# Performance work log

Measured on AMD Instinct MI355X. Metric: run time of the kernel, lower is better.

The kernel has to match this reference:

```python
import jax, jax.numpy as jnp
import numpy as np

DIM = 2048
N_HEADS = 16
KV_HEADS = 2
HEAD_DIM = DIM // N_HEADS
N_REP = N_HEADS // KV_HEADS
EPS = 1e-6


def rms_norm(x, weight):
    # norm over last dim in float32, cast back (inputs already fp32 here)
    xf = x.astype(jnp.float32)
    n = xf * jax.lax.rsqrt(jnp.mean(xf * xf, axis=-1, keepdims=True) + EPS)
    return (weight * n).astype(x.dtype)


def rotate_half(x):
    x1, x2 = jnp.split(x, 2, axis=-1)
    return jnp.concatenate((-x2, x1), axis=-1)


def apply_rotary(x, cos, sin):
    return x * cos + rotate_half(x) * sin


def setup_inputs() -> dict:
    key = jax.random.key(0)
    ks = jax.random.split(key, 8)
    B, S = 2, 2048
    x = jax.random.normal(ks[0], (B, S, DIM), dtype=jnp.float32)
    cos = jax.random.uniform(ks[1], (1, 1, S, HEAD_DIM), dtype=jnp.float32)
    sin = jax.random.uniform(ks[2], (1, 1, S, HEAD_DIM), dtype=jnp.float32)
    scale = 0.02
    wq = jax.random.normal(ks[3], (N_HEADS * HEAD_DIM, DIM), dtype=jnp.float32) * scale
    wk = jax.random.normal(ks[4], (KV_HEADS * HEAD_DIM, DIM), dtype=jnp.float32) * scale
    wv = jax.random.normal(ks[5], (KV_HEADS * HEAD_DIM, DIM), dtype=jnp.float32) * scale
    wo = jax.random.normal(ks[6], (DIM, N_HEADS * HEAD_DIM), dtype=jnp.float32) * scale
    q_gamma = jnp.ones((HEAD_DIM,), dtype=jnp.float32)
    k_gamma = jnp.ones((HEAD_DIM,), dtype=jnp.float32)
    return {"x": x, "cos": cos, "sin": sin, "wq": wq, "wk": wk, "wv": wv,
            "wo": wo, "q_gamma": q_gamma, "k_gamma": k_gamma,
            "signal_token_num": 256}


def reference(x, cos, sin, wq, wk, wv, wo, q_gamma, k_gamma, signal_token_num):
    B, S, D = x.shape
    p = signal_token_num
    # projections (Linear with no bias: x @ W.T)
    xq = (x @ wq.T).reshape(B, S, N_HEADS, HEAD_DIM)
    xk = (x @ wk.T).reshape(B, S, KV_HEADS, HEAD_DIM)
    xv = (x @ wv.T).reshape(B, S, KV_HEADS, HEAD_DIM)
    # QK RMSNorm per head_dim
    xq = rms_norm(xq, q_gamma)
    xk = rms_norm(xk, k_gamma)
    # repeat kv heads (GQA) then [B,H,S,hd]
    xk = jnp.repeat(xk, N_REP, axis=2)
    xv = jnp.repeat(xv, N_REP, axis=2)
    xq = xq.transpose(0, 2, 1, 3)
    xk = xk.transpose(0, 2, 1, 3)
    xv = xv.transpose(0, 2, 1, 3)
    # rotary: original applies identical cos/sin to [:p] and [p:] slices == full apply
    xq = apply_rotary(xq, cos, sin)
    xk = apply_rotary(xk, cos, sin)
    # causal mask with bidirectional prefix block [:p,:p]
    i = jnp.arange(S)[:, None]
    j = jnp.arange(S)[None, :]
    mask = (j <= i) | ((i < p) & (j < p))  # [S,S] bool
    scale = 1.0 / np.sqrt(HEAD_DIM)
    scores = jnp.einsum('bhqd,bhkd->bhqk', xq, xk) * scale
    scores = jnp.where(mask, scores, jnp.finfo(scores.dtype).min)
    attn = jax.nn.softmax(scores, axis=-1)
    out = jnp.einsum('bhqk,bhkd->bhqd', attn, xv)  # [B,H,S,hd]
    out = out.transpose(0, 2, 1, 3).reshape(B, S, N_HEADS * HEAD_DIM)
    return out @ wo.T
```

## Files before the change

kernel.cpp:

```cpp
#include <hip/hip_runtime.h>
#include <stdint.h>

#define S_LEN 2048
#define DIMM  2048
#define NH    16
#define NKV   2

typedef __attribute__((ext_vector_type(8)))  short s16x8;
typedef __attribute__((ext_vector_type(8)))  unsigned short u16x8;
typedef __attribute__((ext_vector_type(4)))  float f32x4;
typedef __attribute__((ext_vector_type(16))) float f32x16;
typedef __attribute__((ext_vector_type(4)))  unsigned int u32x4;

__device__ __forceinline__ unsigned short f2bf(float f){
  unsigned int u = __builtin_bit_cast(unsigned int, f);
  u += 0x7fffu + ((u >> 16) & 1u);
  return (unsigned short)(u >> 16);
}

__device__ __forceinline__ unsigned int cvtpk(float lo, float hi){
  unsigned int r;
  asm("v_cvt_pk_bf16_f32 %0, %1, %2" : "=v"(r) : "v"(lo), "v"(hi));
  return r;
}

__device__ __forceinline__ void gload16(const void* g, void* l){
  __builtin_amdgcn_global_load_lds(
      (const __attribute__((address_space(1))) unsigned int*)g,
      (__attribute__((address_space(3))) unsigned int*)l, 16, 0, 0);
}

__global__ __launch_bounds__(256) void cvt_bf16(const float* __restrict__ src,
                                                unsigned short* __restrict__ dst, int n){
  int i = (blockIdx.x * 256 + threadIdx.x) * 8;
  if (i >= n) return;
  const float4* s4 = (const float4*)(src + i);
  float4 a = s4[0], b = s4[1];
  u16x8 o;
  o[0]=f2bf(a.x); o[1]=f2bf(a.y); o[2]=f2bf(a.z); o[3]=f2bf(a.w);
  o[4]=f2bf(b.x); o[5]=f2bf(b.y); o[6]=f2bf(b.z); o[7]=f2bf(b.w);
  *(u16x8*)(dst + i) = o;
}

__global__ __launch_bounds__(256) void gemm_bt(const unsigned short* __restrict__ A,
                                               const unsigned short* __restrict__ W,
                                               float* __restrict__ C,
                                               int M, int N, int K){
  __shared__ __attribute__((aligned(16))) unsigned short As[128*64];
  __shared__ __attribute__((aligned(16))) unsigned short Bs[128*64];
  const int t = threadIdx.x;
  const int lane = t & 63, wave = t >> 6;
  const int l15 = lane & 15, g = lane >> 4;
  const int lid = blockIdx.y * gridDim.x + blockIdx.x;
  const int cpx = (gridDim.x * gridDim.y) >> 3;
  const int swz = (lid & 7) * cpx + (lid >> 3);
  const int m0 = (swz / gridDim.x) * 128, n0 = (swz % gridDim.x) * 128;
  const int wm = (wave >> 1) * 64, wn = (wave & 1) * 64;
  const int srow = t >> 3, sdblk = t & 7;
  const long ldsoff = (long)(t >> 6) * 1024;
  f32x4 acc[4][4] = {};
  for (int k0 = 0; k0 < K; k0 += 64){
    __syncthreads();
    #pragma unroll
    for (int r = 0; r < 4; ++r){
      int row = r*32 + srow;
      int db  = sdblk ^ (row & 7);
      gload16(A + (long)(m0+row)*K + k0 + db*8, (char*)As + r*4096 + ldsoff);
    }
    #pragma unroll
    for (int r = 0; r < 4; ++r){
      int row = r*32 + srow;
      int db  = sdblk ^ (row & 7);
      gload16(W + (long)(n0+row)*K + k0 + db*8, (char*)Bs + r*4096 + ldsoff);
    }
    __syncthreads();
    s16x8 af[4][2], bfr[4][2];
    #pragma unroll
    for (int mi = 0; mi < 4; ++mi)
      #pragma unroll
      for (int kc = 0; kc < 2; ++kc){
        int row = wm + mi*16 + l15;
        int db = (kc*4 + g) ^ (row & 7);
        af[mi][kc] = *(const s16x8*)(As + row*64 + db*8);
      }
    #pragma unroll
    for (int ni = 0; ni < 4; ++ni)
      #pragma unroll
      for (int kc = 0; kc < 2; ++kc){
        int row = wn + ni*16 + l15;
        int db = (kc*4 + g) ^ (row & 7);
        bfr[ni][kc] = *(const s16x8*)(Bs + row*64 + db*8);
      }
    #pragma unroll
    for (int mi = 0; mi < 4; ++mi)
      #pragma unroll
      for (int ni = 0; ni < 4; ++ni)
        #pragma unroll
        for (int kc = 0; kc < 2; ++kc)
          acc[mi][ni] = __builtin_amdgcn_mfma_f32_16x16x32_bf16(af[mi][kc], bfr[ni][kc], acc[mi][ni], 0, 0, 0);
  }
  #pragma unroll
  for (int mi = 0; mi < 4; ++mi)
    #pragma unroll
    for (int ni = 0; ni < 4; ++ni)
      #pragma unroll
      for (int rg = 0; rg < 4; ++rg){
        int row = m0 + wm + mi*16 + g*4 + rg;
        int col = n0 + wn + ni*16 + l15;
        C[(long)row*N + col] = acc[mi][ni][rg];
      }
}

__global__ __launch_bounds__(256) void normrope(const float* __restrict__ qkv,
    const float* __restrict__ cosb, const float* __restrict__ sinb,
    const float* __restrict__ qg, const float* __restrict__ kg,
    unsigned short* __restrict__ q_attn, unsigned short* __restrict__ k_attn){
  int wave = threadIdx.x >> 6, lane = threadIdx.x & 63;
  int rid = blockIdx.x * 4 + wave;
  int d0 = lane * 2;
  const float* src; unsigned short* dst; const float* gm; float sc; int s;
  if (rid < 2*S_LEN*NH){
    int bs = rid >> 4, h = rid & 15;
    int b = bs >> 11; s = bs & 2047;
    src = qkv + (long)bs*2560 + h*128;
    dst = q_attn + ((long)(b*NH + h)*S_LEN + s)*128;
    gm = qg; sc = 0.08838834764831845f * 1.4426950408889634f;
  } else {
    int r2 = rid - 2*S_LEN*NH;
    int bs = r2 >> 1, kv = r2 & 1;
    int b = bs >> 11; s = bs & 2047;
    src = qkv + (long)bs*2560 + 2048 + kv*128;
    dst = k_attn + ((long)(b*NKV + kv)*S_LEN + s)*128;
    gm = kg; sc = 1.0f;
  }
  float2 x = *(const float2*)(src + d0);
  float ss = x.x*x.x + x.y*x.y;
  #pragma unroll
  for (int m = 1; m < 64; m <<= 1) ss += __shfl_xor(ss, m);
  float r = rsqrtf(ss * (1.0f/128.0f) + 1e-6f);
  float2 gv = *(const float2*)(gm + d0);
  float n0 = x.x * r * gv.x, n1 = x.y * r * gv.y;
  float p0 = __shfl_xor(n0, 32), p1 = __shfl_xor(n1, 32);
  float sgn = (d0 < 64) ? -1.f : 1.f;
  float2 c  = *(const float2*)(cosb + (long)s*128 + d0);
  float2 sn = *(const float2*)(sinb + (long)s*128 + d0);
  float o0 = (n0*c.x + sgn*p0*sn.x) * sc;
  float o1 = (n1*c.y + sgn*p1*sn.y) * sc;
  unsigned int pk = (unsigned int)f2bf(o0) | ((unsigned int)f2bf(o1) << 16);
  *(unsigned int*)(dst + d0) = pk;
}

__global__ __launch_bounds__(256) void vtrans(const float* __restrict__ qkv,
                                              unsigned short* __restrict__ v_t){
  __shared__ __attribute__((aligned(16))) unsigned short lds[128*72];
  int bid = blockIdx.x;
  int s0 = (bid & 31) * 64;
  int kv = (bid >> 5) & 1;
  int b  = bid >> 6;
  int t = threadIdx.x;
  #pragma unroll
  for (int it = 0; it < 32; ++it){
    int idx = it*256 + t;
    int s = idx >> 7, d = idx & 127;
    float v = qkv[(long)(b*S_LEN + s0 + s)*2560 + 2304 + kv*128 + d];
    lds[d*72 + s] = f2bf(v);
  }
  __syncthreads();
  #pragma unroll
  for (int it = 0; it < 4; ++it){
    int c = it*256 + t;
    int d = c >> 3, s8 = c & 7;
    u16x8 vv = *(const u16x8*)(lds + d*72 + s8*8);
    *(u16x8*)(v_t + ((long)(b*NKV + kv)*128 + d)*S_LEN + s0 + s8*8) = vv;
  }
}

__global__ __launch_bounds__(256, 2) void attn_fwd(const unsigned short* __restrict__ q_attn,
    const unsigned short* __restrict__ k_attn, const unsigned short* __restrict__ v_t,
    unsigned short* __restrict__ attn_out, const int* __restrict__ pp){
  __shared__ __attribute__((aligned(16))) unsigned short Ks[2][64*128];
  const int p = pp[0];
  int bid = blockIdx.x;
  int qsb = 15 - (bid >> 5);
  int bh = bid & 31;
  int h = bh & 15, b = bh >> 4;
  int kvh = h >> 3;
  int t = threadIdx.x, wave = t >> 6, lane = t & 63;
  int l31 = lane & 31, hi = lane >> 5;
  int QS = qsb * 128;
  int qw0 = QS + wave*32;
  const int q = qw0 + l31;
  const unsigned short* qb = q_attn + ((long)(b*NH + h)*S_LEN + q)*128 + hi*8;
  s16x8 qf[8];
  #pragma unroll
  for (int m = 0; m < 8; ++m) qf[m] = *(const s16x8*)(qb + m*16);
  f32x16 O[4] = {};
  float mr = -3e38f, lr = 0.f;
  int kvend_w = (qw0 + 31 < p) ? ((p > qw0 + 32) ? p : qw0 + 32) : (qw0 + 32);
  int n_w = (kvend_w + 63) >> 6;
  int kvend_b = (QS + 127 < p) ? ((p > QS + 128) ? p : QS + 128) : (QS + 128);
  int n_blk = (kvend_b + 63) >> 6;
  const unsigned short* kb0 = k_attn + ((long)(b*NKV + kvh)*S_LEN)*128;
  const unsigned short* vb0 = v_t + ((long)(b*NKV + kvh)*128)*S_LEN;
  const int srow = t >> 4, sunit = t & 15;
  const long ldsoff = (long)wave * 1024;
  const unsigned short* vbase = vb0 + (long)l31*S_LEN + hi*8;

  #pragma unroll
  for (int r = 0; r < 4; ++r){
    int row = r*16 + srow;
    int un  = sunit ^ (row & 15);
    gload16(kb0 + (long)row*128 + un*8, (char*)Ks[0] + r*4096 + ldsoff);
  }
  __syncthreads();
  int buf = 0;

  #pragma unroll 1
  for (int ti = 0; ti < n_blk; ++ti){
    int j0 = ti * 64;
    bool act = ti < n_w;
    s16x8 vfA[2][4], vfB[2][4];
    if (act){
      #pragma unroll
      for (int dt = 0; dt < 2; ++dt)
        #pragma unroll
        for (int km = 0; km < 4; ++km)
          vfA[dt][km] = *(const s16x8*)(vbase + (long)dt*32*S_LEN + j0 + km*16);
    }
    if (ti + 1 < n_blk){
      const unsigned short* kb = kb0 + (long)(j0 + 64)*128;
      char* dst = (char*)Ks[buf^1] + ldsoff;
      #pragma unroll
      for (int r = 0; r < 4; ++r){
        int row = r*16 + srow;
        int un  = sunit ^ (row & 15);
        gload16(kb + (long)row*128 + un*8, dst + r*4096);
      }
    }
    if (act){
      const unsigned short* ksc = Ks[buf];
      f32x16 sa[2] = {};
      __builtin_amdgcn_s_setprio(1);
      #pragma unroll
      for (int kt = 0; kt < 2; ++kt){
        int row = kt*32 + l31;
        #pragma unroll
        for (int m = 0; m < 8; ++m){
          int un = (2*m + hi) ^ (row & 15);
          s16x8 kf = *(const s16x8*)(ksc + row*128 + un*8);
          sa[kt] = __builtin_amdgcn_mfma_f32_32x32x16_bf16(kf, qf[m], sa[kt], 0, 0, 0);
        }
      }
      __builtin_amdgcn_s_setprio(0);
      #pragma unroll
      for (int dt = 0; dt < 2; ++dt)
        #pragma unroll
        for (int km = 0; km < 4; ++km)
          vfB[dt][km] = *(const s16x8*)(vbase + (long)(dt+2)*32*S_LEN + j0 + km*16);
      float tm = -3e38f;
      bool full = (j0 + 63 <= qw0) || ((qw0 + 31 < p) && (j0 + 63 < p));
      if (full){
        #pragma unroll
        for (int kt = 0; kt < 2; ++kt)
          #pragma unroll
          for (int rg = 0; rg < 16; ++rg) tm = fmaxf(tm, sa[kt][rg]);
      } else {
        #pragma unroll
        for (int kt = 0; kt < 2; ++kt)
          #pragma unroll
          for (int rg = 0; rg < 16; ++rg){
            int j = j0 + kt*32 + (rg & 3) + 8*(rg >> 2) + 4*hi;
            bool ok = (j <= q) || ((q < p) && (j < p));
            float sv = ok ? sa[kt][rg] : -3e38f;
            sa[kt][rg] = sv;
            tm = fmaxf(tm, sv);
          }
      }
      tm = fmaxf(tm, __shfl_xor(tm, 32));
      if (!__all(tm <= mr + 8.0f)){
        float nm = fmaxf(mr, tm);
        float sfv = exp2f(mr - nm);
        mr = nm;
        lr *= sfv;
        float sfO[16];
        #pragma unroll
        for (int rg = 0; rg < 16; ++rg){
          int qr = (rg & 3) + 8*(rg >> 2) + 4*hi;
          sfO[rg] = __shfl(sfv, qr | (lane & 32));
        }
        #pragma unroll
        for (int dt = 0; dt < 4; ++dt)
          #pragma unroll
          for (int rg = 0; rg < 16; ++rg) O[dt][rg] *= sfO[rg];
      }
      float rs = 0.f;
      #pragma unroll
      for (int kt = 0; kt < 2; ++kt)
        #pragma unroll
        for (int rg = 0; rg < 16; ++rg){
          float e = exp2f(sa[kt][rg] - mr);
          sa[kt][rg] = e;
          rs += e;
        }
      rs += __shfl_xor(rs, 32);
      lr += rs;
      __builtin_amdgcn_s_setprio(1);
      #pragma unroll
      for (int km = 0; km < 4; ++km){
        int base = (km & 1) * 8;
        const f32x16& s = sa[km >> 1];
        unsigned int a0 = cvtpk(s[base+0], s[base+1]);
        unsigned int b0 = cvtpk(s[base+4], s[base+5]);
        asm("v_permlane32_swap_b32 %0, %1" : "+v"(a0), "+v"(b0));
        unsigned int a1 = cvtpk(s[base+2], s[base+3]);
        unsigned int b1 = cvtpk(s[base+6], s[base+7]);
        asm("v_permlane32_swap_b32 %0, %1" : "+v"(a1), "+v"(b1));
        u32x4 w; w[0] = a0; w[1] = a1; w[2] = b0; w[3] = b1;
        s16x8 pf = __builtin_bit_cast(s16x8, w);
        #pragma unroll
        for (int dt = 0; dt < 2; ++dt)
          O[dt] = __builtin_amdgcn_mfma_f32_32x32x16_bf16(pf, vfA[dt][km], O[dt], 0, 0, 0);
        #pragma unroll
        for (int dt = 2; dt < 4; ++dt)
          O[dt] = __builtin_amdgcn_mfma_f32_32x32x16_bf16(pf, vfB[dt-2][km], O[dt], 0, 0, 0);
      }
      __builtin_amdgcn_s_setprio(0);
    }
    __syncthreads();
    buf ^= 1;
  }
  float inv = 1.0f / lr;
  float invO[16];
  #pragma unroll
  for (int rg = 0; rg < 16; ++rg){
    int qr = (rg & 3) + 8*(rg >> 2) + 4*hi;
    invO[rg] = __shfl(inv, qr | (lane & 32));
  }
  #pragma unroll
  for (int dt = 0; dt < 4; ++dt)
    #pragma unroll
    for (int rg = 0; rg < 16; ++rg){
      int row = qw0 + (rg & 3) + 8*(rg >> 2) + 4*hi;
      int col = h*128 + dt*32 + l31;
      attn_out[(long)(b*S_LEN + row)*DIMM + col] = f2bf(O[dt][rg]*invO[rg]);
    }
}

extern "C" void kernel_launch(void* const* d_in, const int* in_sizes, int n_in,
                              void* d_out, int out_size, void* d_ws, size_t ws_size,
                              hipStream_t stream){
  const float* x    = (const float*)d_in[0];
  const float* cosb = (const float*)d_in[1];
  const float* sinb = (const float*)d_in[2];
  const float* wq   = (const float*)d_in[3];
  const float* wk   = (const float*)d_in[4];
  const float* wv   = (const float*)d_in[5];
  const float* wo   = (const float*)d_in[6];
  const float* qg   = (const float*)d_in[7];
  const float* kg   = (const float*)d_in[8];
  const int*   pp   = (const int*)d_in[9];

  char* ws = (char*)d_ws;
  unsigned short* xb    = (unsigned short*)(ws);
  unsigned short* wqkvb = (unsigned short*)(ws + 16777216);
  unsigned short* wob   = (unsigned short*)(ws + 27262976);
  float*          qkv   = (float*)(ws + 35651584);
  unsigned short* qat   = (unsigned short*)(ws + 77594624);
  unsigned short* kat   = (unsigned short*)(ws + 94371840);
  unsigned short* vt    = (unsigned short*)(ws + 96468992);
  unsigned short* aout  = (unsigned short*)(ws + 98566144);

  cvt_bf16<<<8388608/2048, 256, 0, stream>>>(x,  xb, 8388608);
  cvt_bf16<<<4194304/2048, 256, 0, stream>>>(wq, wqkvb, 4194304);
  cvt_bf16<<< 524288/2048, 256, 0, stream>>>(wk, wqkvb + 4194304, 524288);
  cvt_bf16<<< 524288/2048, 256, 0, stream>>>(wv, wqkvb + 4718592, 524288);
  cvt_bf16<<<4194304/2048, 256, 0, stream>>>(wo, wob, 4194304);

  gemm_bt<<<dim3(2560/128, 4096/128), 256, 0, stream>>>(xb, wqkvb, qkv, 4096, 2560, 2048);
  normrope<<<73728/4, 256, 0, stream>>>(qkv, cosb, sinb, qg, kg, qat, kat);
  vtrans<<<128, 256, 0, stream>>>(qkv, vt);
  attn_fwd<<<512, 256, 0, stream>>>(qat, kat, vt, aout, pp);
  gemm_bt<<<dim3(2048/128, 4096/128), 256, 0, stream>>>(aout, wob, (float*)d_out, 4096, 2048, 2048);
}
```

Measured before the change: 266.7 us.

## Split KV range for long causal query blocks and merge partial results

```diff
diff --git a/kernel.cpp b/kernel.cpp
--- a/kernel.cpp
+++ b/kernel.cpp
@@ -177,12 +177,24 @@
 
 __global__ __launch_bounds__(256, 2) void attn_fwd(const unsigned short* __restrict__ q_attn,
     const unsigned short* __restrict__ k_attn, const unsigned short* __restrict__ v_t,
-    unsigned short* __restrict__ attn_out, const int* __restrict__ pp){
+    unsigned short* __restrict__ attn_out, float* __restrict__ part,
+    const int* __restrict__ pp){
   __shared__ __attribute__((aligned(16))) unsigned short Ks[2][64*128];
   const int p = pp[0];
   int bid = blockIdx.x;
-  int qsb = 15 - (bid >> 5);
-  int bh = bid & 31;
+  int qsb, bh, chunk; bool split;
+  if (bid < 512){
+    split = true;
+    qsb = 15 - (bid >> 6);
+    chunk = (bid >> 5) & 1;
+    bh = bid & 31;
+  } else {
+    split = false;
+    int e = bid - 512;
+    qsb = e >> 5;
+    chunk = 0;
+    bh = e & 31;
+  }
   int h = bh & 15, b = bh >> 4;
   int kvh = h >> 3;
   int t = threadIdx.x, wave = t >> 6, lane = t & 63;
@@ -200,23 +212,28 @@
   int n_w = (kvend_w + 63) >> 6;
   int kvend_b = (QS + 127 < p) ? ((p > QS + 128) ? p : QS + 128) : (QS + 128);
   int n_blk = (kvend_b + 63) >> 6;
+  int tbeg = (split && chunk) ? (n_blk >> 1) : 0;
+  int tend = split ? (chunk ? n_blk : (n_blk >> 1)) : n_blk;
   const unsigned short* kb0 = k_attn + ((long)(b*NKV + kvh)*S_LEN)*128;
   const unsigned short* vb0 = v_t + ((long)(b*NKV + kvh)*128)*S_LEN;
   const int srow = t >> 4, sunit = t & 15;
   const long ldsoff = (long)wave * 1024;
   const unsigned short* vbase = vb0 + (long)l31*S_LEN + hi*8;
 
-  #pragma unroll
-  for (int r = 0; r < 4; ++r){
-    int row = r*16 + srow;
-    int un  = sunit ^ (row & 15);
-    gload16(kb0 + (long)row*128 + un*8, (char*)Ks[0] + r*4096 + ldsoff);
+  {
+    const unsigned short* kb = kb0 + (long)(tbeg*64)*128;
+    #pragma unroll
+    for (int r = 0; r < 4; ++r){
+      int row = r*16 + srow;
+      int un  = sunit ^ (row & 15);
+      gload16(kb + (long)row*128 + un*8, (char*)Ks[0] + r*4096 + ldsoff);
+    }
   }
   __syncthreads();
   int buf = 0;
 
   #pragma unroll 1
-  for (int ti = 0; ti < n_blk; ++ti){
+  for (int ti = tbeg; ti < tend; ++ti){
     int j0 = ti * 64;
     bool act = ti < n_w;
     s16x8 vfA[2][4], vfB[2][4];
@@ -227,7 +244,7 @@
         for (int km = 0; km < 4; ++km)
           vfA[dt][km] = *(const s16x8*)(vbase + (long)dt*32*S_LEN + j0 + km*16);
     }
-    if (ti + 1 < n_blk){
+    if (ti + 1 < tend){
       const unsigned short* kb = kb0 + (long)(j0 + 64)*128;
       char* dst = (char*)Ks[buf^1] + ldsoff;
       #pragma unroll
@@ -329,21 +346,74 @@
     __syncthreads();
     buf ^= 1;
   }
-  float inv = 1.0f / lr;
-  float invO[16];
-  #pragma unroll
-  for (int rg = 0; rg < 16; ++rg){
-    int qr = (rg & 3) + 8*(rg >> 2) + 4*hi;
-    invO[rg] = __shfl(inv, qr | (lane & 32));
-  }
-  #pragma unroll
-  for (int dt = 0; dt < 4; ++dt)
+
+  if (!split){
+    float inv = 1.0f / lr;
+    float invO[16];
     #pragma unroll
     for (int rg = 0; rg < 16; ++rg){
-      int row = qw0 + (rg & 3) + 8*(rg >> 2) + 4*hi;
-      int col = h*128 + dt*32 + l31;
-      attn_out[(long)(b*S_LEN + row)*DIMM + col] = f2bf(O[dt][rg]*invO[rg]);
-    }
+      int qr = (rg & 3) + 8*(rg >> 2) + 4*hi;
+      invO[rg] = __shfl(inv, qr | (lane & 32));
+    }
+    #pragma unroll
+    for (int dt = 0; dt < 4; ++dt)
+      #pragma unroll
+      for (int rg = 0; rg < 16; ++rg){
+        int row = qw0 + (rg & 3) + 8*(rg >> 2) + 4*hi;
+        int col = h*128 + dt*32 + l31;
+        attn_out[(long)(b*S_LEN + row)*DIMM + col] = f2bf(O[dt][rg]*invO[rg]);
+      }
+  } else {
+    float* pb = part + ((((long)b*NH + h)*8 + (qsb - 8))*2 + chunk) * 16640;
+    #pragma unroll
+    for (int dt = 0; dt < 4; ++dt)
+      #pragma unroll
+      for (int rg = 0; rg < 16; ++rg){
+        int rowl = wave*32 + (rg & 3) + 8*(rg >> 2) + 4*hi;
+        pb[(long)rowl*128 + dt*32 + l31] = O[dt][rg];
+      }
+    if (hi == 0){
+      pb[16384 + (wave*32 + l31)*2 + 0] = mr;
+      pb[16384 + (wave*32 + l31)*2 + 1] = lr;
+    }
+  }
+}
+
+__global__ __launch_bounds__(256) void attn_merge(const float* __restrict__ part,
+                                                  unsigned short* __restrict__ attn_out){
+  int bid = blockIdx.x;
+  int si = bid >> 5;
+  int bh = bid & 31;
+  int h = bh & 15, b = bh >> 4;
+  const float* p0 = part + ((((long)b*NH + h)*8 + si)*2 + 0) * 16640;
+  const float* p1 = p0 + 16640;
+  int t = threadIdx.x;
+  int r = t >> 1, ch = t & 1;
+  float m0 = p0[16384 + r*2], l0 = p0[16384 + r*2 + 1];
+  float m1 = p1[16384 + r*2], l1 = p1[16384 + r*2 + 1];
+  float m  = fmaxf(m0, m1);
+  float s0 = exp2f(m0 - m), s1 = exp2f(m1 - m);
+  float inv = 1.0f / (l0*s0 + l1*s1);
+  float a0 = s0*inv, a1 = s1*inv;
+  int row = (8 + si)*128 + r;
+  const float4* x0 = (const float4*)(p0 + (long)r*128 + ch*64);
+  const float4* x1 = (const float4*)(p1 + (long)r*128 + ch*64);
+  unsigned short* w = attn_out + (long)(b*S_LEN + row)*DIMM + h*128 + ch*64;
+  #pragma unroll
+  for (int i = 0; i < 8; ++i){
+    float4 ya = x0[2*i],   yb = x0[2*i+1];
+    float4 za = x1[2*i],   zb = x1[2*i+1];
+    u16x8 o;
+    o[0] = f2bf(ya.x*a0 + za.x*a1);
+    o[1] = f2bf(ya.y*a0 + za.y*a1);
+    o[2] = f2bf(ya.z*a0 + za.z*a1);
+    o[3] = f2bf(ya.w*a0 + za.w*a1);
+    o[4] = f2bf(yb.x*a0 + zb.x*a1);
+    o[5] = f2bf(yb.y*a0 + zb.y*a1);
+    o[6] = f2bf(yb.z*a0 + zb.z*a1);
+    o[7] = f2bf(yb.w*a0 + zb.w*a1);
+    *(u16x8*)(w + i*8) = o;
+  }
 }
 
 extern "C" void kernel_launch(void* const* d_in, const int* in_sizes, int n_in,
@@ -369,6 +439,7 @@
   unsigned short* kat   = (unsigned short*)(ws + 94371840);
   unsigned short* vt    = (unsigned short*)(ws + 96468992);
   unsigned short* aout  = (unsigned short*)(ws + 98566144);
+  float*          part  = (float*)(ws + 35651584);
 
   cvt_bf16<<<8388608/2048, 256, 0, stream>>>(x,  xb, 8388608);
   cvt_bf16<<<4194304/2048, 256, 0, stream>>>(wq, wqkvb, 4194304);
@@ -379,6 +450,7 @@
   gemm_bt<<<dim3(2560/128, 4096/128), 256, 0, stream>>>(xb, wqkvb, qkv, 4096, 2560, 2048);
   normrope<<<73728/4, 256, 0, stream>>>(qkv, cosb, sinb, qg, kg, qat, kat);
   vtrans<<<128, 256, 0, stream>>>(qkv, vt);
-  attn_fwd<<<512, 256, 0, stream>>>(qat, kat, vt, aout, pp);
+  attn_fwd<<<768, 256, 0, stream>>>(qat, kat, vt, aout, part, pp);
+  attn_merge<<<256, 256, 0, stream>>>(part, aout);
   gemm_bt<<<dim3(2048/128, 4096/128), 256, 0, stream>>>(aout, wob, (float*)d_out, 4096, 2048, 2048);
 }
```

After: 273.6 us. +2.6%, slower.

## Emit bf16 QKV from projection GEMM and load K directly from global in attention

Applied to the files above, without the earlier changes.

```diff
diff --git a/kernel.cpp b/kernel.cpp
--- a/kernel.cpp
+++ b/kernel.cpp
@@ -16,6 +16,10 @@
   unsigned int u = __builtin_bit_cast(unsigned int, f);
   u += 0x7fffu + ((u >> 16) & 1u);
   return (unsigned short)(u >> 16);
+}
+
+__device__ __forceinline__ float bf2f(unsigned short u){
+  return __builtin_bit_cast(float, ((unsigned int)u) << 16);
 }
 
 __device__ __forceinline__ unsigned int cvtpk(float lo, float hi){
@@ -42,9 +46,10 @@
   *(u16x8*)(dst + i) = o;
 }
 
+template<bool OBF16>
 __global__ __launch_bounds__(256) void gemm_bt(const unsigned short* __restrict__ A,
                                                const unsigned short* __restrict__ W,
-                                               float* __restrict__ C,
+                                               void* __restrict__ Cv,
                                                int M, int N, int K){
   __shared__ __attribute__((aligned(16))) unsigned short As[128*64];
   __shared__ __attribute__((aligned(16))) unsigned short Bs[128*64];
@@ -107,18 +112,21 @@
       for (int rg = 0; rg < 4; ++rg){
         int row = m0 + wm + mi*16 + g*4 + rg;
         int col = n0 + wn + ni*16 + l15;
-        C[(long)row*N + col] = acc[mi][ni][rg];
-      }
-}
-
-__global__ __launch_bounds__(256) void normrope(const float* __restrict__ qkv,
+        if (OBF16)
+          ((unsigned short*)Cv)[(long)row*N + col] = f2bf(acc[mi][ni][rg]);
+        else
+          ((float*)Cv)[(long)row*N + col] = acc[mi][ni][rg];
+      }
+}
+
+__global__ __launch_bounds__(256) void normrope(const unsigned short* __restrict__ qkv,
     const float* __restrict__ cosb, const float* __restrict__ sinb,
     const float* __restrict__ qg, const float* __restrict__ kg,
     unsigned short* __restrict__ q_attn, unsigned short* __restrict__ k_attn){
   int wave = threadIdx.x >> 6, lane = threadIdx.x & 63;
   int rid = blockIdx.x * 4 + wave;
   int d0 = lane * 2;
-  const float* src; unsigned short* dst; const float* gm; float sc; int s;
+  const unsigned short* src; unsigned short* dst; const float* gm; float sc; int s;
   if (rid < 2*S_LEN*NH){
     int bs = rid >> 4, h = rid & 15;
     int b = bs >> 11; s = bs & 2047;
@@ -133,13 +141,15 @@
     dst = k_attn + ((long)(b*NKV + kv)*S_LEN + s)*128;
     gm = kg; sc = 1.0f;
   }
-  float2 x = *(const float2*)(src + d0);
-  float ss = x.x*x.x + x.y*x.y;
+  unsigned int xw = *(const unsigned int*)(src + d0);
+  float x0 = bf2f((unsigned short)(xw & 0xffff));
+  float x1 = bf2f((unsigned short)(xw >> 16));
+  float ss = x0*x0 + x1*x1;
   #pragma unroll
   for (int m = 1; m < 64; m <<= 1) ss += __shfl_xor(ss, m);
   float r = rsqrtf(ss * (1.0f/128.0f) + 1e-6f);
   float2 gv = *(const float2*)(gm + d0);
-  float n0 = x.x * r * gv.x, n1 = x.y * r * gv.y;
+  float n0 = x0 * r * gv.x, n1 = x1 * r * gv.y;
   float p0 = __shfl_xor(n0, 32), p1 = __shfl_xor(n1, 32);
   float sgn = (d0 < 64) ? -1.f : 1.f;
   float2 c  = *(const float2*)(cosb + (long)s*128 + d0);
@@ -150,7 +160,7 @@
   *(unsigned int*)(dst + d0) = pk;
 }
 
-__global__ __launch_bounds__(256) void vtrans(const float* __restrict__ qkv,
+__global__ __launch_bounds__(256) void vtrans(const unsigned short* __restrict__ qkv,
                                               unsigned short* __restrict__ v_t){
   __shared__ __attribute__((aligned(16))) unsigned short lds[128*72];
   int bid = blockIdx.x;
@@ -162,8 +172,7 @@
   for (int it = 0; it < 32; ++it){
     int idx = it*256 + t;
     int s = idx >> 7, d = idx & 127;
-    float v = qkv[(long)(b*S_LEN + s0 + s)*2560 + 2304 + kv*128 + d];
-    lds[d*72 + s] = f2bf(v);
+    lds[d*72 + s] = qkv[(long)(b*S_LEN + s0 + s)*2560 + 2304 + kv*128 + d];
   }
   __syncthreads();
   #pragma unroll
@@ -175,10 +184,9 @@
   }
 }
 
-__global__ __launch_bounds__(256, 2) void attn_fwd(const unsigned short* __restrict__ q_attn,
+__global__ __launch_bounds__(256) void attn_fwd(const unsigned short* __restrict__ q_attn,
     const unsigned short* __restrict__ k_attn, const unsigned short* __restrict__ v_t,
     unsigned short* __restrict__ attn_out, const int* __restrict__ pp){
-  __shared__ __attribute__((aligned(16))) unsigned short Ks[2][64*128];
   const int p = pp[0];
   int bid = blockIdx.x;
   int qsb = 15 - (bid >> 5);
@@ -198,136 +206,105 @@
   float mr = -3e38f, lr = 0.f;
   int kvend_w = (qw0 + 31 < p) ? ((p > qw0 + 32) ? p : qw0 + 32) : (qw0 + 32);
   int n_w = (kvend_w + 63) >> 6;
-  int kvend_b = (QS + 127 < p) ? ((p > QS + 128) ? p : QS + 128) : (QS + 128);
-  int n_blk = (kvend_b + 63) >> 6;
   const unsigned short* kb0 = k_attn + ((long)(b*NKV + kvh)*S_LEN)*128;
   const unsigned short* vb0 = v_t + ((long)(b*NKV + kvh)*128)*S_LEN;
-  const int srow = t >> 4, sunit = t & 15;
-  const long ldsoff = (long)wave * 1024;
   const unsigned short* vbase = vb0 + (long)l31*S_LEN + hi*8;
-
-  #pragma unroll
-  for (int r = 0; r < 4; ++r){
-    int row = r*16 + srow;
-    int un  = sunit ^ (row & 15);
-    gload16(kb0 + (long)row*128 + un*8, (char*)Ks[0] + r*4096 + ldsoff);
-  }
-  __syncthreads();
-  int buf = 0;
+  const unsigned short* kbase = kb0 + (long)l31*128 + hi*8;
 
   #pragma unroll 1
-  for (int ti = 0; ti < n_blk; ++ti){
+  for (int ti = 0; ti < n_w; ++ti){
     int j0 = ti * 64;
-    bool act = ti < n_w;
     s16x8 vfA[2][4], vfB[2][4];
-    if (act){
-      #pragma unroll
-      for (int dt = 0; dt < 2; ++dt)
+    #pragma unroll
+    for (int dt = 0; dt < 2; ++dt)
+      #pragma unroll
+      for (int km = 0; km < 4; ++km)
+        vfA[dt][km] = *(const s16x8*)(vbase + (long)dt*32*S_LEN + j0 + km*16);
+    f32x16 sa[2] = {};
+    __builtin_amdgcn_s_setprio(1);
+    #pragma unroll
+    for (int kt = 0; kt < 2; ++kt){
+      const unsigned short* krow = kbase + (long)(j0 + kt*32)*128;
+      #pragma unroll
+      for (int m = 0; m < 8; ++m){
+        s16x8 kf = *(const s16x8*)(krow + m*16);
+        sa[kt] = __builtin_amdgcn_mfma_f32_32x32x16_bf16(kf, qf[m], sa[kt], 0, 0, 0);
+      }
+    }
+    __builtin_amdgcn_s_setprio(0);
+    #pragma unroll
+    for (int dt = 0; dt < 2; ++dt)
+      #pragma unroll
+      for (int km = 0; km < 4; ++km)
+        vfB[dt][km] = *(const s16x8*)(vbase + (long)(dt+2)*32*S_LEN + j0 + km*16);
+    float tm = -3e38f;
+    bool full = (j0 + 63 <= qw0) || ((qw0 + 31 < p) && (j0 + 63 < p));
+    if (full){
+      #pragma unroll
+      for (int kt = 0; kt < 2; ++kt)
         #pragma unroll
-        for (int km = 0; km < 4; ++km)
-          vfA[dt][km] = *(const s16x8*)(vbase + (long)dt*32*S_LEN + j0 + km*16);
-    }
-    if (ti + 1 < n_blk){
-      const unsigned short* kb = kb0 + (long)(j0 + 64)*128;
-      char* dst = (char*)Ks[buf^1] + ldsoff;
-      #pragma unroll
-      for (int r = 0; r < 4; ++r){
-        int row = r*16 + srow;
-        int un  = sunit ^ (row & 15);
-        gload16(kb + (long)row*128 + un*8, dst + r*4096);
-      }
-    }
-    if (act){
-      const unsigned short* ksc = Ks[buf];
-      f32x16 sa[2] = {};
-      __builtin_amdgcn_s_setprio(1);
-      #pragma unroll
-      for (int kt = 0; kt < 2; ++kt){
-        int row = kt*32 + l31;
-        #pragma unroll
-        for (int m = 0; m < 8; ++m){
-          int un = (2*m + hi) ^ (row & 15);
-          s16x8 kf = *(const s16x8*)(ksc + row*128 + un*8);
-          sa[kt] = __builtin_amdgcn_mfma_f32_32x32x16_bf16(kf, qf[m], sa[kt], 0, 0, 0);
-        }
-      }
-      __builtin_amdgcn_s_setprio(0);
-      #pragma unroll
-      for (int dt = 0; dt < 2; ++dt)
-        #pragma unroll
-        for (int km = 0; km < 4; ++km)
-          vfB[dt][km] = *(const s16x8*)(vbase + (long)(dt+2)*32*S_LEN + j0 + km*16);
-      float tm = -3e38f;
-      bool full = (j0 + 63 <= qw0) || ((qw0 + 31 < p) && (j0 + 63 < p));
-      if (full){
-        #pragma unroll
-        for (int kt = 0; kt < 2; ++kt)
-          #pragma unroll
-          for (int rg = 0; rg < 16; ++rg) tm = fmaxf(tm, sa[kt][rg]);
-      } else {
-        #pragma unroll
-        for (int kt = 0; kt < 2; ++kt)
-          #pragma unroll
-          for (int rg = 0; rg < 16; ++rg){
-            int j = j0 + kt*32 + (rg & 3) + 8*(rg >> 2) + 4*hi;
-            bool ok = (j <= q) || ((q < p) && (j < p));
-            float sv = ok ? sa[kt][rg] : -3e38f;
-            sa[kt][rg] = sv;
-            tm = fmaxf(tm, sv);
-          }
-      }
-      tm = fmaxf(tm, __shfl_xor(tm, 32));
-      if (!__all(tm <= mr + 8.0f)){
-        float nm = fmaxf(mr, tm);
-        float sfv = exp2f(mr - nm);
-        mr = nm;
-        lr *= sfv;
-        float sfO[16];
-        #pragma unroll
-        for (int rg = 0; rg < 16; ++rg){
-          int qr = (rg & 3) + 8*(rg >> 2) + 4*hi;
-          sfO[rg] = __shfl(sfv, qr | (lane & 32));
-        }
-        #pragma unroll
-        for (int dt = 0; dt < 4; ++dt)
-          #pragma unroll
-          for (int rg = 0; rg < 16; ++rg) O[dt][rg] *= sfO[rg];
-      }
-      float rs = 0.f;
+        for (int rg = 0; rg < 16; ++rg) tm = fmaxf(tm, sa[kt][rg]);
+    } else {
       #pragma unroll
       for (int kt = 0; kt < 2; ++kt)
         #pragma unroll
         for (int rg = 0; rg < 16; ++rg){
-          float e = exp2f(sa[kt][rg] - mr);
-          sa[kt][rg] = e;
-          rs += e;
+          int j = j0 + kt*32 + (rg & 3) + 8*(rg >> 2) + 4*hi;
+          bool ok = (j <= q) || ((q < p) && (j < p));
+          float sv = ok ? sa[kt][rg] : -3e38f;
+          sa[kt][rg] = sv;
+          tm = fmaxf(tm, sv);
         }
-      rs += __shfl_xor(rs, 32);
-      lr += rs;
-      __builtin_amdgcn_s_setprio(1);
-      #pragma unroll
-      for (int km = 0; km < 4; ++km){
-        int base = (km & 1) * 8;
-        const f32x16& s = sa[km >> 1];
-        unsigned int a0 = cvtpk(s[base+0], s[base+1]);
-        unsigned int b0 = cvtpk(s[base+4], s[base+5]);
-        asm("v_permlane32_swap_b32 %0, %1" : "+v"(a0), "+v"(b0));
-        unsigned int a1 = cvtpk(s[base+2], s[base+3]);
-        unsigned int b1 = cvtpk(s[base+6], s[base+7]);
-        asm("v_permlane32_swap_b32 %0, %1" : "+v"(a1), "+v"(b1));
-        u32x4 w; w[0] = a0; w[1] = a1; w[2] = b0; w[3] = b1;
-        s16x8 pf = __builtin_bit_cast(s16x8, w);
+    }
+    tm = fmaxf(tm, __shfl_xor(tm, 32));
+    if (!__all(tm <= mr + 8.0f)){
+      float nm = fmaxf(mr, tm);
+      float sfv = exp2f(mr - nm);
+      mr = nm;
+      lr *= sfv;
+      float sfO[16];
+      #pragma unroll
+      for (int rg = 0; rg < 16; ++rg){
+        int qr = (rg & 3) + 8*(rg >> 2) + 4*hi;
+        sfO[rg] = __shfl(sfv, qr | (lane & 32));
+      }
+      #pragma unroll
+      for (int dt = 0; dt < 4; ++dt)
         #pragma unroll
-        for (int dt = 0; dt < 2; ++dt)
-          O[dt] = __builtin_amdgcn_mfma_f32_32x32x16_bf16(pf, vfA[dt][km], O[dt], 0, 0, 0);
-        #pragma unroll
-        for (int dt = 2; dt < 4; ++dt)
-          O[dt] = __builtin_amdgcn_mfma_f32_32x32x16_bf16(pf, vfB[dt-2][km], O[dt], 0, 0, 0);
-      }
-      __builtin_amdgcn_s_setprio(0);
-    }
-    __syncthreads();
-    buf ^= 1;
+        for (int rg = 0; rg < 16; ++rg) O[dt][rg] *= sfO[rg];
+    }
+    float rs = 0.f;
+    #pragma unroll
+    for (int kt = 0; kt < 2; ++kt)
+      #pragma unroll
+      for (int rg = 0; rg < 16; ++rg){
+        float e = exp2f(sa[kt][rg] - mr);
+        sa[kt][rg] = e;
+        rs += e;
+      }
+    rs += __shfl_xor(rs, 32);
+    lr += rs;
+    __builtin_amdgcn_s_setprio(1);
+    #pragma unroll
+    for (int km = 0; km < 4; ++km){
+      int base = (km & 1) * 8;
+      const f32x16& s = sa[km >> 1];
+      unsigned int a0 = cvtpk(s[base+0], s[base+1]);
+      unsigned int b0 = cvtpk(s[base+4], s[base+5]);
+      asm("v_permlane32_swap_b32 %0, %1" : "+v"(a0), "+v"(b0));
+      unsigned int a1 = cvtpk(s[base+2], s[base+3]);
+      unsigned int b1 = cvtpk(s[base+6], s[base+7]);
+      asm("v_permlane32_swap_b32 %0, %1" : "+v"(a1), "+v"(b1));
+      u32x4 w; w[0] = a0; w[1] = a1; w[2] = b0; w[3] = b1;
+      s16x8 pf = __builtin_bit_cast(s16x8, w);
+      #pragma unroll
+      for (int dt = 0; dt < 2; ++dt)
+        O[dt] = __builtin_amdgcn_mfma_f32_32x32x16_bf16(pf, vfA[dt][km], O[dt], 0, 0, 0);
+      #pragma unroll
+      for (int dt = 2; dt < 4; ++dt)
+        O[dt] = __builtin_amdgcn_mfma_f32_32x32x16_bf16(pf, vfB[dt-2][km], O[dt], 0, 0, 0);
+    }
+    __builtin_amdgcn_s_setprio(0);
   }
   float inv = 1.0f / lr;
   float invO[16];
@@ -364,7 +341,7 @@
   unsigned short* xb    = (unsigned short*)(ws);
   unsigned short* wqkvb = (unsigned short*)(ws + 16777216);
   unsigned short* wob   = (unsigned short*)(ws + 27262976);
-  float*          qkv   = (float*)(ws + 35651584);
+  unsigned short* qkvb  = (unsigned short*)(ws + 35651584);
   unsigned short* qat   = (unsigned short*)(ws + 77594624);
   unsigned short* kat   = (unsigned short*)(ws + 94371840);
   unsigned short* vt    = (unsigned short*)(ws + 96468992);
@@ -376,9 +353,9 @@
   cvt_bf16<<< 524288/2048, 256, 0, stream>>>(wv, wqkvb + 4718592, 524288);
   cvt_bf16<<<4194304/2048, 256, 0, stream>>>(wo, wob, 4194304);
 
-  gemm_bt<<<dim3(2560/128, 4096/128), 256, 0, stream>>>(xb, wqkvb, qkv, 4096, 2560, 2048);
-  normrope<<<73728/4, 256, 0, stream>>>(qkv, cosb, sinb, qg, kg, qat, kat);
-  vtrans<<<128, 256, 0, stream>>>(qkv, vt);
+  gemm_bt<true><<<dim3(2560/128, 4096/128), 256, 0, stream>>>(xb, wqkvb, qkvb, 4096, 2560, 2048);
+  normrope<<<73728/4, 256, 0, stream>>>(qkvb, cosb, sinb, qg, kg, qat, kat);
+  vtrans<<<128, 256, 0, stream>>>(qkvb, vt);
   attn_fwd<<<512, 256, 0, stream>>>(qat, kat, vt, aout, pp);
-  gemm_bt<<<dim3(2048/128, 4096/128), 256, 0, stream>>>(aout, wob, (float*)d_out, 4096, 2048, 2048);
-}
+  gemm_bt<false><<<dim3(2048/128, 4096/128), 256, 0, stream>>>(aout, wob, d_out, 4096, 2048, 2048);
+}
```

After: 288.6 us. 8.2% more time.
